# Kernel optimization log

Hardware: AMD Instinct MI355X
Metric: run time of the kernel (lower is better)

The kernel has to match this reference:

```python
import jax, jax.numpy as jnp
import numpy as np

B = 64          # number of graphs in the batch
NK = 262144     # total known (branch) nodes
NC = 262144     # total query (trunk) nodes
F = 3           # in_feats (3D coordinates)
H = 256         # hidden_size
O = 3           # out_feats


def _linear_init(key, fan_in, fan_out):
    s = 1.0 / np.sqrt(fan_in)
    kw, kb = jax.random.split(key)
    w = jax.random.uniform(kw, (fan_in, fan_out), minval=-s, maxval=s, dtype=jnp.float32)
    b = jax.random.uniform(kb, (fan_out,), minval=-s, maxval=s, dtype=jnp.float32)
    return w, b


def _mlp3(x, w0, b0, w1, b1, w2, b2):
    h = jax.nn.relu(x @ w0 + b0)
    h = jax.nn.relu(h @ w1 + b1)
    return h @ w2 + b2


def setup_inputs() -> dict:
    key = jax.random.key(0)
    ks = jax.random.split(key, 12)
    known_nodes = jax.random.normal(ks[0], (NK, F), dtype=jnp.float32)
    nodes = jax.random.normal(ks[1], (NC, F), dtype=jnp.float32)
    known_seg = jnp.sort(jax.random.randint(ks[2], (NK,), 0, B)).astype(jnp.int32)
    coord_seg = jnp.sort(jax.random.randint(ks[3], (NC,), 0, B)).astype(jnp.int32)
    # branch (Node_Classification approximated as 3-layer MLP)
    bw0, bb0 = _linear_init(ks[4], F, H)
    bw1, bb1 = _linear_init(ks[5], H, H)
    bw2, bb2 = _linear_init(ks[6], H, H)
    # trunk
    tw0, tb0 = _linear_init(ks[7], F, H)
    tw1, tb1 = _linear_init(ks[8], H, H)
    tw2, tb2 = _linear_init(ks[9], H, H)
    # out head
    ow0, ob0 = _linear_init(ks[10], H, H)
    ow1, ob1 = _linear_init(ks[11], H, O)
    return dict(known_nodes=known_nodes, nodes=nodes, known_seg=known_seg,
                coord_seg=coord_seg,
                bw0=bw0, bb0=bb0, bw1=bw1, bb1=bb1, bw2=bw2, bb2=bb2,
                tw0=tw0, tb0=tb0, tw1=tw1, tb1=tb1, tw2=tw2, tb2=tb2,
                ow0=ow0, ob0=ob0, ow1=ow1, ob1=ob1)


def reference(known_nodes, nodes, known_seg, coord_seg,
              bw0, bb0, bw1, bb1, bw2, bb2,
              tw0, tb0, tw1, tb1, tw2, tb2,
              ow0, ob0, ow1, ob1):
    # branch: per known-node features [NK, H]
    f = _mlp3(known_nodes, bw0, bb0, bw1, bb1, bw2, bb2)
    # trunk: per query-node features [NC, H]
    c = _mlp3(nodes, tw0, tb0, tw1, tb1, tw2, tb2)
    # c[None]*f[:,None] then mean over query axis == f * segment_mean(c)
    seg_sum = jax.ops.segment_sum(c, coord_seg, num_segments=B)        # [B, H]
    cnt = jax.ops.segment_sum(jnp.ones((c.shape[0], 1), c.dtype), coord_seg,
                              num_segments=B)                          # [B, 1]
    seg_mean = seg_sum / jnp.maximum(cnt, 1.0)
    feat = f * seg_mean[known_seg]                                     # [NK, H]
    h = jax.nn.relu(feat @ ow0 + ob0)
    return h @ ow1 + ob1                                               # [NK, O]
```

## Files before the change

kernel.cpp:

```cpp
#include <hip/hip_runtime.h>

#define HH 256
#define NB 64
#define ROWS 64
#define NTOT 262144
#define THREADS 256

typedef _Float16 half8 __attribute__((ext_vector_type(8)));
typedef _Float16 half4 __attribute__((ext_vector_type(4)));
typedef float f32x4 __attribute__((ext_vector_type(4)));

typedef __attribute__((address_space(1))) const void gas_t;
typedef __attribute__((address_space(3))) void las_t;

__device__ __forceinline__ uint32_t swz(uint32_t r, uint32_t k) {
  return (((r << 9) + (k << 1)) ^ ((r & 7) << 4)) ^ ((r & 8) << 3);
}

__device__ __forceinline__ void stage_slab(const char* __restrict__ g, char* l,
                                           int lane)
{
  const char* gp = g + lane * 16;
#pragma unroll
  for (int c = 0; c < 4; ++c)
    __builtin_amdgcn_global_load_lds((gas_t*)(gp + c * 1024), (las_t*)(l + c * 1024),
                                     16, 0, 0);
}

template<int MODE>
__device__ __forceinline__ void heavy_layer(char* act, char* wpan,
                                            const char* __restrict__ wt3,
                                            const float* __restrict__ bias,
                                            const float* __restrict__ seg_mean,
                                            const int* __restrict__ seg_g, int tid)
{
  const int wid  = tid >> 6;
  const int lane = tid & 63;
  const int lr   = lane & 15;
  const int lg   = lane >> 4;
  const int j0   = wid << 6;
  char* slab = wpan + wid * 12288;
  const char* wsrc = wt3 + wid * 4096;

  f32x4 acc[4][4];
#pragma unroll
  for (int jf = 0; jf < 4; ++jf)
#pragma unroll
    for (int rf = 0; rf < 4; ++rf)
      acc[jf][rf] = (f32x4){0.f, 0.f, 0.f, 0.f};

  stage_slab(wsrc + 0 * 16384, slab + 0 * 4096, lane);
  stage_slab(wsrc + 1 * 16384, slab + 1 * 4096, lane);
  stage_slab(wsrc + 2 * 16384, slab + 2 * 4096, lane);

  half8 a[2][4], b[2][4];

  asm volatile("s_waitcnt vmcnt(8)" ::: "memory");
  __builtin_amdgcn_sched_barrier(0);
#pragma unroll
  for (int rf = 0; rf < 4; ++rf)
    b[0][rf] = *(const half8*)(act + swz(rf * 16 + lr, 0 * 32 + lg * 8));
#pragma unroll
  for (int jf = 0; jf < 4; ++jf)
    a[0][jf] = *(const half8*)(slab + 0 * 4096 + jf * 1024 + lane * 16);

#pragma unroll
  for (int ks = 0; ks < 8; ++ks) {
    const int p = ks & 1;
    if (ks < 7) {
      if (ks < 6) asm volatile("s_waitcnt vmcnt(4)" ::: "memory");
      else        asm volatile("s_waitcnt vmcnt(0)" ::: "memory");
      __builtin_amdgcn_sched_barrier(0);
#pragma unroll
      for (int rf = 0; rf < 4; ++rf)
        b[p ^ 1][rf] = *(const half8*)(act + swz(rf * 16 + lr, (ks + 1) * 32 + lg * 8));
#pragma unroll
      for (int jf = 0; jf < 4; ++jf)
        a[p ^ 1][jf] = *(const half8*)(slab + ((ks + 1) % 3) * 4096 + jf * 1024 + lane * 16);
    }
    __builtin_amdgcn_sched_barrier(0);
#pragma unroll
    for (int jf = 0; jf < 4; ++jf)
#pragma unroll
      for (int rf = 0; rf < 4; ++rf)
        acc[jf][rf] = __builtin_amdgcn_mfma_f32_16x16x32_f16(a[p][jf], b[p][rf], acc[jf][rf], 0, 0, 0);
    __builtin_amdgcn_sched_barrier(0);
    if (ks < 5)
      stage_slab(wsrc + (ks + 3) * 16384, slab + (ks % 3) * 4096, lane);
  }

  int sseg[4];
  if (MODE == 2) {
#pragma unroll
    for (int rf = 0; rf < 4; ++rf) sseg[rf] = seg_g[rf * 16 + lr];
  }

  __syncthreads();

#pragma unroll
  for (int jf = 0; jf < 4; ++jf) {
    f32x4 bj = *(const f32x4*)(bias + j0 + jf * 16 + lg * 4);
#pragma unroll
    for (int rf = 0; rf < 4; ++rf) {
      f32x4 v = acc[jf][rf] + bj;
      if (MODE == 2) {
        f32x4 sm = *(const f32x4*)(seg_mean + sseg[rf] * HH + j0 + jf * 16 + lg * 4);
        v *= sm;
      }
      half4 h;
#pragma unroll
      for (int u = 0; u < 4; ++u) {
        float x = v[u];
        if (MODE == 0) x = fmaxf(x, 0.f);
        h[u] = (_Float16)x;
      }
      *(half4*)(act + swz(rf * 16 + lr, j0 + jf * 16 + lg * 4)) = h;
    }
  }
  __syncthreads();
}

__device__ __forceinline__ void layer1_mfma(char* act, const float* __restrict__ x,
                                            int r0g, const float* __restrict__ W0,
                                            const float* __restrict__ b0, int tid)
{
  const int wid  = tid >> 6;
  const int lane = tid & 63;
  const int lr   = lane & 15;
  const int lg   = lane >> 4;
  const int j0   = wid << 6;

  half8 a[4];
#pragma unroll
  for (int jf = 0; jf < 4; ++jf) {
    half8 v = {0, 0, 0, 0, 0, 0, 0, 0};
    if (lg == 0) {
      int j = j0 + jf * 16 + lr;
      v[0] = (_Float16)W0[j];
      v[1] = (_Float16)W0[HH + j];
      v[2] = (_Float16)W0[2 * HH + j];
    }
    a[jf] = v;
  }

  f32x4 acc[4][4];
#pragma unroll
  for (int jf = 0; jf < 4; ++jf)
#pragma unroll
    for (int rf = 0; rf < 4; ++rf)
      acc[jf][rf] = (f32x4){0.f, 0.f, 0.f, 0.f};

#pragma unroll
  for (int rf = 0; rf < 4; ++rf) {
    half8 b = {0, 0, 0, 0, 0, 0, 0, 0};
    if (lg == 0) {
      const float* xp = x + (size_t)(r0g + rf * 16 + lr) * 3;
      b[0] = (_Float16)xp[0];
      b[1] = (_Float16)xp[1];
      b[2] = (_Float16)xp[2];
    }
#pragma unroll
    for (int jf = 0; jf < 4; ++jf)
      acc[jf][rf] = __builtin_amdgcn_mfma_f32_16x16x32_f16(a[jf], b, acc[jf][rf], 0, 0, 0);
  }

#pragma unroll
  for (int jf = 0; jf < 4; ++jf) {
    f32x4 bj = *(const f32x4*)(b0 + j0 + jf * 16 + lg * 4);
#pragma unroll
    for (int rf = 0; rf < 4; ++rf) {
      f32x4 v = acc[jf][rf] + bj;
      half4 h;
#pragma unroll
      for (int u = 0; u < 4; ++u)
        h[u] = (_Float16)fmaxf(v[u], 0.f);
      *(half4*)(act + swz(rf * 16 + lr, j0 + jf * 16 + lg * 4)) = h;
    }
  }
  __syncthreads();
}

__global__ __launch_bounds__(THREADS, 2)
void trunk_kernel(const float* __restrict__ nodes, const int* __restrict__ coord_seg,
                  const float* __restrict__ tw0, const float* __restrict__ tb0,
                  const char* __restrict__ wt3_1, const float* __restrict__ tb1,
                  const char* __restrict__ wt3_2, const float* __restrict__ tb2,
                  float* __restrict__ seg_sum)
{
  __shared__ __align__(16) char act[ROWS * HH * 2];
  __shared__ __align__(16) char wpan[4 * 12288];
  const int tid = threadIdx.x;
  const int r0g = blockIdx.x * ROWS;

  layer1_mfma(act, nodes, r0g, tw0, tb0, tid);
  heavy_layer<0>(act, wpan, wt3_1, tb1, nullptr, nullptr, tid);
  heavy_layer<1>(act, wpan, wt3_2, tb2, nullptr, nullptr, tid);

  {
    const int j = tid;
    const int s_lo = coord_seg[r0g];
    const int s_hi = coord_seg[r0g + ROWS - 1];
    if (s_lo == s_hi) {
      float p = 0.f;
#pragma unroll 8
      for (int r = 0; r < ROWS; ++r)
        p += (float)*(const _Float16*)(act + swz(r, j));
      atomicAdd(&seg_sum[s_lo * HH + j], p);
    } else {
      for (int s = s_lo; s <= s_hi; ++s) {
        float p = 0.f;
        for (int r = 0; r < ROWS; ++r)
          if (coord_seg[r0g + r] == s)
            p += (float)*(const _Float16*)(act + swz(r, j));
        atomicAdd(&seg_sum[s * HH + j], p);
      }
    }
  }
}

__global__ void dbias_kernel(const float* __restrict__ seg_mean,
                             const float* __restrict__ bb2,
                             const float* __restrict__ ow0,
                             const float* __restrict__ ob0,
                             float* __restrict__ d_s)
{
  const int s = blockIdx.x, j = threadIdx.x;
  float acc = ob0[j];
  for (int i = 0; i < HH; ++i)
    acc = fmaf(bb2[i] * seg_mean[s * HH + i], ow0[i * HH + j], acc);
  d_s[s * HH + j] = acc;
}

__global__ __launch_bounds__(THREADS, 2)
void cfuse_kernel(const float* __restrict__ bw2, const float* __restrict__ seg_mean,
                  const char* __restrict__ wt3_ow0, char* __restrict__ Cbuf)
{
  __shared__ __align__(16) char act[ROWS * HH * 2];
  __shared__ __align__(16) char wpan[4 * 12288];
  const int tid = threadIdx.x;
  const int s  = blockIdx.x >> 2;
  const int kc = blockIdx.x & 3;
  const int k0 = kc * 64;

  {
    const int i = tid;
    const float mi = seg_mean[s * HH + i];
    for (int r = 0; r < ROWS; ++r)
      *(_Float16*)(act + swz(r, i)) = (_Float16)(bw2[(size_t)(k0 + r) * HH + i] * mi);
  }
  __syncthreads();

  const int wid  = tid >> 6;
  const int lane = tid & 63;
  const int lr   = lane & 15;
  const int lg   = lane >> 4;
  const int j0   = wid << 6;
  char* slab = wpan + wid * 12288;
  const char* wsrc = wt3_ow0 + wid * 4096;

  f32x4 acc[4][4];
#pragma unroll
  for (int jf = 0; jf < 4; ++jf)
#pragma unroll
    for (int rf = 0; rf < 4; ++rf)
      acc[jf][rf] = (f32x4){0.f, 0.f, 0.f, 0.f};

  stage_slab(wsrc + 0 * 16384, slab + 0 * 4096, lane);
  stage_slab(wsrc + 1 * 16384, slab + 1 * 4096, lane);
  stage_slab(wsrc + 2 * 16384, slab + 2 * 4096, lane);

  half8 a[2][4], b[2][4];
  asm volatile("s_waitcnt vmcnt(8)" ::: "memory");
  __builtin_amdgcn_sched_barrier(0);
#pragma unroll
  for (int rf = 0; rf < 4; ++rf)
    b[0][rf] = *(const half8*)(act + swz(rf * 16 + lr, 0 * 32 + lg * 8));
#pragma unroll
  for (int jf = 0; jf < 4; ++jf)
    a[0][jf] = *(const half8*)(slab + 0 * 4096 + jf * 1024 + lane * 16);

#pragma unroll
  for (int ks = 0; ks < 8; ++ks) {
    const int p = ks & 1;
    if (ks < 7) {
      if (ks < 6) asm volatile("s_waitcnt vmcnt(4)" ::: "memory");
      else        asm volatile("s_waitcnt vmcnt(0)" ::: "memory");
      __builtin_amdgcn_sched_barrier(0);
#pragma unroll
      for (int rf = 0; rf < 4; ++rf)
        b[p ^ 1][rf] = *(const half8*)(act + swz(rf * 16 + lr, (ks + 1) * 32 + lg * 8));
#pragma unroll
      for (int jf = 0; jf < 4; ++jf)
        a[p ^ 1][jf] = *(const half8*)(slab + ((ks + 1) % 3) * 4096 + jf * 1024 + lane * 16);
    }
    __builtin_amdgcn_sched_barrier(0);
#pragma unroll
    for (int jf = 0; jf < 4; ++jf)
#pragma unroll
      for (int rf = 0; rf < 4; ++rf)
        acc[jf][rf] = __builtin_amdgcn_mfma_f32_16x16x32_f16(a[p][jf], b[p][rf], acc[jf][rf], 0, 0, 0);
    __builtin_amdgcn_sched_barrier(0);
    if (ks < 5)
      stage_slab(wsrc + (ks + 3) * 16384, slab + (ks % 3) * 4096, lane);
  }

  char* dbuf = wpan;
#pragma unroll
  for (int jf = 0; jf < 4; ++jf)
#pragma unroll
    for (int rf = 0; rf < 4; ++rf) {
      const int kl = rf * 16 + lr;
#pragma unroll
      for (int u = 0; u < 4; ++u) {
        const int j = j0 + jf * 16 + lg * 4 + u;
        *(_Float16*)(dbuf + j * 128 + ((kl * 2) ^ ((j & 7) << 4))) = (_Float16)acc[jf][rf][u];
      }
    }
  __syncthreads();

  char* Cdst = Cbuf + (size_t)s * 131072 + (size_t)(kc * 2) * 16384;
#pragma unroll
  for (int c = 0; c < 8; ++c) {
    const uint32_t g = c * 4096 + tid * 16;
    const uint32_t sl = g >> 14;
    const uint32_t aa = g & 16383;
    const uint32_t wq = aa >> 12;
    const uint32_t jjf = (aa >> 10) & 3;
    const uint32_t l  = (aa >> 4) & 63;
    const uint32_t j  = wq * 64 + jjf * 16 + (l & 15);
    const uint32_t kl = sl * 32 + ((l >> 4) << 3);
    uint4 v = *(const uint4*)(dbuf + j * 128 + ((kl * 2) ^ ((j & 7) << 4)));
    *(uint4*)(Cdst + sl * 16384 + aa) = v;
  }
}

__global__ __launch_bounds__(THREADS, 2)
void branch_kernel(const float* __restrict__ known_nodes, const int* __restrict__ known_seg,
                   const float* __restrict__ bw0, const float* __restrict__ bb0,
                   const char* __restrict__ wt3_1, const float* __restrict__ bb1,
                   const char* __restrict__ wt3_2, const float* __restrict__ bb2,
                   const float* __restrict__ seg_mean,
                   const char* __restrict__ wt3_o, const float* __restrict__ ob0,
                   const float* __restrict__ ow1, const float* __restrict__ ob1,
                   const char* __restrict__ Cbuf, const float* __restrict__ d_s,
                   int use_fuse, float* __restrict__ out)
{
  __shared__ __align__(16) char act[ROWS * HH * 2];
  __shared__ __align__(16) char wpan[4 * 12288];
  const int tid = threadIdx.x;
  const int bid = ((int)blockIdx.x & 7) * ((int)gridDim.x >> 3) + ((int)blockIdx.x >> 3);
  const int r0g = bid * ROWS;

  layer1_mfma(act, known_nodes, r0g, bw0, bb0, tid);
  heavy_layer<0>(act, wpan, wt3_1, bb1, nullptr, nullptr, tid);

  const int s_lo = known_seg[r0g];
  const int s_hi = known_seg[r0g + ROWS - 1];
  if (use_fuse && s_lo == s_hi) {
    heavy_layer<0>(act, wpan, Cbuf + (size_t)s_lo * 131072, d_s + s_lo * HH,
                   nullptr, nullptr, tid);
  } else {
    heavy_layer<2>(act, wpan, wt3_2, bb2, seg_mean, known_seg + r0g, tid);
    heavy_layer<0>(act, wpan, wt3_o, ob0, nullptr, nullptr, tid);
  }

  float* ps = (float*)wpan;
  {
    const int r = tid & 63;
    const int q = tid >> 6;
    float o0 = 0.f, o1 = 0.f, o2 = 0.f;
    for (int kk = 0; kk < 64; kk += 8) {
      int k0 = q * 64 + kk;
      half8 h = *(const half8*)(act + swz(r, k0));
#pragma unroll
      for (int u = 0; u < 8; ++u) {
        float a = (float)h[u];
        o0 = fmaf(a, ow1[(k0 + u) * 3 + 0], o0);
        o1 = fmaf(a, ow1[(k0 + u) * 3 + 1], o1);
        o2 = fmaf(a, ow1[(k0 + u) * 3 + 2], o2);
      }
    }
    float* p = ps + q * ROWS * 3;
    p[r * 3 + 0] = o0; p[r * 3 + 1] = o1; p[r * 3 + 2] = o2;
  }
  __syncthreads();
  if (tid < ROWS) {
    const int r = tid;
    float* dst = out + (size_t)(r0g + r) * 3;
#pragma unroll
    for (int c = 0; c < 3; ++c) {
      float o = ob1[c];
#pragma unroll
      for (int q = 0; q < 4; ++q) o += ps[q * ROWS * 3 + r * 3 + c];
      dst[c] = o;
    }
  }
}

struct WPtrs { const float* w[5]; char* wt3[5]; };
__global__ void transpose_kernel(WPtrs p)
{
  const int m = blockIdx.x >> 8;
  const int k = blockIdx.x & 255;
  const int j = threadIdx.x;
  size_t off = (size_t)(k >> 5) * 16384 + (size_t)(j >> 6) * 4096
             + (size_t)((j >> 4) & 3) * 1024
             + (size_t)((((k >> 3) & 3) << 4) | (j & 15)) * 16
             + (size_t)(k & 7) * 2;
  *(_Float16*)(p.wt3[m] + off) = (_Float16)p.w[m][k * HH + j];
}

__global__ void zero_kernel(float* __restrict__ p, int n)
{
  int i = blockIdx.x * blockDim.x + threadIdx.x;
  if (i < n) p[i] = 0.f;
}

__global__ void mean_kernel(const float* __restrict__ seg_sum,
                            const int* __restrict__ coord_seg,
                            float* __restrict__ seg_mean)
{
  const int b = blockIdx.x;
  int lo = 0, n = NTOT;
  while (n > 0) { int h = n >> 1; int mid = lo + h;
    if (coord_seg[mid] < b) { lo = mid + 1; n -= h + 1; } else n = h; }
  int hi = lo; n = NTOT - lo;
  while (n > 0) { int h = n >> 1; int mid = hi + h;
    if (coord_seg[mid] < b + 1) { hi = mid + 1; n -= h + 1; } else n = h; }
  float inv = 1.0f / fmaxf((float)(hi - lo), 1.0f);
  seg_mean[b * HH + threadIdx.x] = seg_sum[b * HH + threadIdx.x] * inv;
}

extern "C" void kernel_launch(void* const* d_in, const int* in_sizes, int n_in,
                              void* d_out, int out_size, void* d_ws, size_t ws_size,
                              hipStream_t stream)
{
  const float* known_nodes = (const float*)d_in[0];
  const float* nodes       = (const float*)d_in[1];
  const int*   known_seg   = (const int*)d_in[2];
  const int*   coord_seg   = (const int*)d_in[3];
  const float* bw0 = (const float*)d_in[4];
  const float* bb0 = (const float*)d_in[5];
  const float* bw1 = (const float*)d_in[6];
  const float* bb1 = (const float*)d_in[7];
  const float* bw2 = (const float*)d_in[8];
  const float* bb2 = (const float*)d_in[9];
  const float* tw0 = (const float*)d_in[10];
  const float* tb0 = (const float*)d_in[11];
  const float* tw1 = (const float*)d_in[12];
  const float* tb1 = (const float*)d_in[13];
  const float* tw2 = (const float*)d_in[14];
  const float* tb2 = (const float*)d_in[15];
  const float* ow0 = (const float*)d_in[16];
  const float* ob0 = (const float*)d_in[17];
  const float* ow1 = (const float*)d_in[18];
  const float* ob1 = (const float*)d_in[19];

  float* out      = (float*)d_out;
  char* p = (char*)d_ws;
  float* seg_sum  = (float*)p;            p += (size_t)NB * HH * 4;
  float* seg_mean = (float*)p;            p += (size_t)NB * HH * 4;
  char* wt3_tw1 = p;  p += (size_t)HH * HH * 2;
  char* wt3_tw2 = p;  p += (size_t)HH * HH * 2;
  char* wt3_bw1 = p;  p += (size_t)HH * HH * 2;
  char* wt3_bw2 = p;  p += (size_t)HH * HH * 2;
  char* wt3_ow0 = p;  p += (size_t)HH * HH * 2;
  float* d_s    = (float*)p;              p += (size_t)NB * HH * 4;
  char* Cbuf    = p;                      p += (size_t)NB * HH * HH * 2;
  const int use_fuse = ((size_t)(p - (char*)d_ws) <= ws_size) ? 1 : 0;

  WPtrs wp;
  wp.w[0] = tw1; wp.wt3[0] = wt3_tw1;
  wp.w[1] = tw2; wp.wt3[1] = wt3_tw2;
  wp.w[2] = bw1; wp.wt3[2] = wt3_bw1;
  wp.w[3] = bw2; wp.wt3[3] = wt3_bw2;
  wp.w[4] = ow0; wp.wt3[4] = wt3_ow0;

  transpose_kernel<<<5 * 256, 256, 0, stream>>>(wp);
  zero_kernel<<<(NB * HH + 255) / 256, 256, 0, stream>>>(seg_sum, NB * HH);
  trunk_kernel<<<NTOT / ROWS, THREADS, 0, stream>>>(nodes, coord_seg,
                                                    tw0, tb0, wt3_tw1, tb1, wt3_tw2, tb2,
                                                    seg_sum);
  mean_kernel<<<NB, 256, 0, stream>>>(seg_sum, coord_seg, seg_mean);
  if (use_fuse) {
    dbias_kernel<<<NB, 256, 0, stream>>>(seg_mean, bb2, ow0, ob0, d_s);
    cfuse_kernel<<<NB * 4, THREADS, 0, stream>>>(bw2, seg_mean, wt3_ow0, Cbuf);
  }
  branch_kernel<<<NTOT / ROWS, THREADS, 0, stream>>>(known_nodes, known_seg,
                                                     bw0, bb0, wt3_bw1, bb1, wt3_bw2, bb2,
                                                     seg_mean,
                                                     wt3_ow0, ob0, ow1, ob1,
                                                     Cbuf, d_s, use_fuse,
                                                     out);
}
```

Baseline: 245.2 us.

## Apply trunk last linear layer after segment reduction instead of per node

The trunk's final layer has no activation, so segment_sum(h W + b) equals segment_sum(h) W + count*b. The trunk kernel now reduces the layer-2 activations per segment and drops its third heavy GEMM. A small segmix kernel applies tw2 and the bias to the 64 segment sums and divides by the count, replacing mean_kernel. This removes about a third of the trunk's matrix work and one weight transpose, at the cost of a small serial per-segment matvec.

Result: faster. 222.8 us (-9.1%).

```diff
diff --git a/kernel.cpp b/kernel.cpp
--- a/kernel.cpp
+++ b/kernel.cpp
@@ -184,8 +184,7 @@
 void trunk_kernel(const float* __restrict__ nodes, const int* __restrict__ coord_seg,
                   const float* __restrict__ tw0, const float* __restrict__ tb0,
                   const char* __restrict__ wt3_1, const float* __restrict__ tb1,
-                  const char* __restrict__ wt3_2, const float* __restrict__ tb2,
-                  float* __restrict__ seg_sum)
+                  float* __restrict__ seg_a)
 {
   __shared__ __align__(16) char act[ROWS * HH * 2];
   __shared__ __align__(16) char wpan[4 * 12288];
@@ -194,7 +193,6 @@
 
   layer1_mfma(act, nodes, r0g, tw0, tb0, tid);
   heavy_layer<0>(act, wpan, wt3_1, tb1, nullptr, nullptr, tid);
-  heavy_layer<1>(act, wpan, wt3_2, tb2, nullptr, nullptr, tid);
 
   {
     const int j = tid;
@@ -205,17 +203,37 @@
 #pragma unroll 8
       for (int r = 0; r < ROWS; ++r)
         p += (float)*(const _Float16*)(act + swz(r, j));
-      atomicAdd(&seg_sum[s_lo * HH + j], p);
+      atomicAdd(&seg_a[s_lo * HH + j], p);
     } else {
       for (int s = s_lo; s <= s_hi; ++s) {
         float p = 0.f;
         for (int r = 0; r < ROWS; ++r)
           if (coord_seg[r0g + r] == s)
             p += (float)*(const _Float16*)(act + swz(r, j));
-        atomicAdd(&seg_sum[s * HH + j], p);
+        atomicAdd(&seg_a[s * HH + j], p);
       }
     }
   }
+}
+
+__global__ void segmix_kernel(const float* __restrict__ seg_a,
+                              const int* __restrict__ coord_seg,
+                              const float* __restrict__ tw2,
+                              const float* __restrict__ tb2,
+                              float* __restrict__ seg_mean)
+{
+  const int s = blockIdx.x, j = threadIdx.x;
+  int lo = 0, n = NTOT;
+  while (n > 0) { int h = n >> 1; int mid = lo + h;
+    if (coord_seg[mid] < s) { lo = mid + 1; n -= h + 1; } else n = h; }
+  int hi = lo; n = NTOT - lo;
+  while (n > 0) { int h = n >> 1; int mid = hi + h;
+    if (coord_seg[mid] < s + 1) { hi = mid + 1; n -= h + 1; } else n = h; }
+  const float cnt = (float)(hi - lo);
+  float acc = cnt * tb2[j];
+  for (int i = 0; i < HH; ++i)
+    acc = fmaf(seg_a[s * HH + i], tw2[i * HH + j], acc);
+  seg_mean[s * HH + j] = acc / fmaxf(cnt, 1.0f);
 }
 
 __global__ void dbias_kernel(const float* __restrict__ seg_mean,
@@ -397,7 +415,7 @@
   }
 }
 
-struct WPtrs { const float* w[5]; char* wt3[5]; };
+struct WPtrs { const float* w[4]; char* wt3[4]; };
 __global__ void transpose_kernel(WPtrs p)
 {
   const int m = blockIdx.x >> 8;
@@ -414,21 +432,6 @@
 {
   int i = blockIdx.x * blockDim.x + threadIdx.x;
   if (i < n) p[i] = 0.f;
-}
-
-__global__ void mean_kernel(const float* __restrict__ seg_sum,
-                            const int* __restrict__ coord_seg,
-                            float* __restrict__ seg_mean)
-{
-  const int b = blockIdx.x;
-  int lo = 0, n = NTOT;
-  while (n > 0) { int h = n >> 1; int mid = lo + h;
-    if (coord_seg[mid] < b) { lo = mid + 1; n -= h + 1; } else n = h; }
-  int hi = lo; n = NTOT - lo;
-  while (n > 0) { int h = n >> 1; int mid = hi + h;
-    if (coord_seg[mid] < b + 1) { hi = mid + 1; n -= h + 1; } else n = h; }
-  float inv = 1.0f / fmaxf((float)(hi - lo), 1.0f);
-  seg_mean[b * HH + threadIdx.x] = seg_sum[b * HH + threadIdx.x] * inv;
 }
 
 extern "C" void kernel_launch(void* const* d_in, const int* in_sizes, int n_in,
@@ -458,10 +461,9 @@
 
   float* out      = (float*)d_out;
   char* p = (char*)d_ws;
-  float* seg_sum  = (float*)p;            p += (size_t)NB * HH * 4;
+  float* seg_a    = (float*)p;            p += (size_t)NB * HH * 4;
   float* seg_mean = (float*)p;            p += (size_t)NB * HH * 4;
   char* wt3_tw1 = p;  p += (size_t)HH * HH * 2;
-  char* wt3_tw2 = p;  p += (size_t)HH * HH * 2;
   char* wt3_bw1 = p;  p += (size_t)HH * HH * 2;
   char* wt3_bw2 = p;  p += (size_t)HH * HH * 2;
   char* wt3_ow0 = p;  p += (size_t)HH * HH * 2;
@@ -471,17 +473,16 @@
 
   WPtrs wp;
   wp.w[0] = tw1; wp.wt3[0] = wt3_tw1;
-  wp.w[1] = tw2; wp.wt3[1] = wt3_tw2;
-  wp.w[2] = bw1; wp.wt3[2] = wt3_bw1;
-  wp.w[3] = bw2; wp.wt3[3] = wt3_bw2;
-  wp.w[4] = ow0; wp.wt3[4] = wt3_ow0;
-
-  transpose_kernel<<<5 * 256, 256, 0, stream>>>(wp);
-  zero_kernel<<<(NB * HH + 255) / 256, 256, 0, stream>>>(seg_sum, NB * HH);
+  wp.w[1] = bw1; wp.wt3[1] = wt3_bw1;
+  wp.w[2] = bw2; wp.wt3[2] = wt3_bw2;
+  wp.w[3] = ow0; wp.wt3[3] = wt3_ow0;
+
+  transpose_kernel<<<4 * 256, 256, 0, stream>>>(wp);
+  zero_kernel<<<(NB * HH + 255) / 256, 256, 0, stream>>>(seg_a, NB * HH);
   trunk_kernel<<<NTOT / ROWS, THREADS, 0, stream>>>(nodes, coord_seg,
-                                                    tw0, tb0, wt3_tw1, tb1, wt3_tw2, tb2,
-                                                    seg_sum);
-  mean_kernel<<<NB, 256, 0, stream>>>(seg_sum, coord_seg, seg_mean);
+                                                    tw0, tb0, wt3_tw1, tb1,
+                                                    seg_a);
+  segmix_kernel<<<NB, 256, 0, stream>>>(seg_a, coord_seg, tw2, tb2, seg_mean);
   if (use_fuse) {
     dbias_kernel<<<NB, 256, 0, stream>>>(seg_mean, bb2, ow0, ob0, d_s);
     cfuse_kernel<<<NB * 4, THREADS, 0, stream>>>(bw2, seg_mean, wt3_ow0, Cbuf);
```
